# Kernel tuning notes

Measured on AMD Instinct MI355X. Metric: run time of the kernel, lower is better.

## Reference

```python
import jax, jax.numpy as jnp
import numpy as np

NODES_PER_GRAPH = 40
NEG_SLOPE = 0.1


def gcn_conv(x, src, dst, deg_inv_sqrt, W, b):
    # PyG GCNConv: h = x @ W.T; symmetric-normalized aggregation with self-loops; + bias
    h = x @ W.T                                   # [N, out]
    norm = deg_inv_sqrt[src] * deg_inv_sqrt[dst]  # [E]
    msgs = h[src] * norm[:, None]                 # [E, out]
    agg = jax.ops.segment_sum(msgs, dst, num_segments=x.shape[0])
    # self-loop contribution: norm_ii = deg_inv_sqrt[i]^2 = 1/deg[i]
    agg = agg + h * (deg_inv_sqrt ** 2)[:, None]
    return agg + b


def setup_inputs() -> dict:
    key = jax.random.key(0)
    ks = jax.random.split(key, 12)
    N, E, C = 200000, 1000000, 40
    hid1, hid2, hid3, lin1, lin2, out = 128, 256, 128, 512, 128, 1

    def glorot(k, shape):
        fan_in = shape[-1]
        return jax.random.normal(k, shape, dtype=jnp.float32) * (1.0 / np.sqrt(fan_in))

    x = jax.random.normal(ks[0], (N, C), dtype=jnp.float32)
    edge_index = jax.random.randint(ks[1], (2, E), 0, N, dtype=jnp.int64)
    return {
        "x": x,
        "edge_index": edge_index,
        "W1": glorot(ks[2], (hid1, C)), "b1": jnp.zeros((hid1,), jnp.float32),
        "W2": glorot(ks[3], (hid2, hid1)), "b2": jnp.zeros((hid2,), jnp.float32),
        "W3": glorot(ks[4], (hid3, hid2)), "b3": jnp.zeros((hid3,), jnp.float32),
        "L1w": glorot(ks[5], (lin1, NODES_PER_GRAPH * hid3)), "L1b": jnp.zeros((lin1,), jnp.float32),
        "L2w": glorot(ks[6], (lin2, lin1)), "L2b": jnp.zeros((lin2,), jnp.float32),
        "L3w": glorot(ks[7], (out, lin2)), "L3b": jnp.zeros((out,), jnp.float32),
    }


def reference(x, edge_index, W1, b1, W2, b2, W3, b3, L1w, L1b, L2w, L2b, L3w, L3b):
    N = x.shape[0]
    src, dst = edge_index[0], edge_index[1]
    # degree with self-loops (edge weight 1), shared by all three convs
    deg = jax.ops.segment_sum(jnp.ones_like(dst, dtype=x.dtype), dst, num_segments=N) + 1.0
    deg_inv_sqrt = jax.lax.rsqrt(deg)

    lrelu = lambda v: jax.nn.leaky_relu(v, NEG_SLOPE)

    h = lrelu(gcn_conv(x, src, dst, deg_inv_sqrt, W1, b1))
    # dropout is identity in eval mode
    h = lrelu(gcn_conv(h, src, dst, deg_inv_sqrt, W2, b2))
    h = lrelu(gcn_conv(h, src, dst, deg_inv_sqrt, W3, b3))

    g = h.reshape(N // NODES_PER_GRAPH, -1)   # [G, 40*hid3]
    g = lrelu(g @ L1w.T + L1b)
    g = lrelu(g @ L2w.T + L2b)
    g = g @ L3w.T + L3b
    return jax.nn.sigmoid(g)                   # [G, 1]
```

## Files before the change

### kernel.cpp

```cpp
#include <hip/hip_runtime.h>
#include <cmath>

#define CDIV(a,b) (((a)+(b)-1)/(b))

typedef unsigned short bf16_t;
using short8 = __attribute__((ext_vector_type(8))) short;
using f32x4  = __attribute__((ext_vector_type(4))) float;
using u16x4  = __attribute__((ext_vector_type(4))) unsigned short;
using u16x8  = __attribute__((ext_vector_type(8))) unsigned short;

__device__ __forceinline__ float bf2f(unsigned short b) {
    unsigned u = ((unsigned)b) << 16;
    float f;
    __builtin_memcpy(&f, &u, 4);
    return f;
}
__device__ __forceinline__ unsigned short f2bf(float f) {
    unsigned u;
    __builtin_memcpy(&u, &f, 4);
    u = (u + 0x7FFFu + ((u >> 16) & 1u)) >> 16;
    return (unsigned short)u;
}

__device__ __forceinline__ void gload16(const bf16_t* g, unsigned short* l) {
    __builtin_amdgcn_global_load_lds(
        (const __attribute__((address_space(1))) void*)(g),
        (__attribute__((address_space(3))) void*)(l), 16, 0, 0);
}

__device__ __forceinline__ int edge_src(const int* ei, int E, int f, int i) {
    return f ? ei[2 * (size_t)i] : ei[i];
}
__device__ __forceinline__ int edge_dst(const int* ei, int E, int f, int i) {
    return f ? ei[2 * ((size_t)E + (size_t)i)] : ei[(size_t)E + (size_t)i];
}

__global__ __launch_bounds__(256) void k_packhist(const int* __restrict__ ei, int E,
                                                  int* __restrict__ src32,
                                                  int* __restrict__ dst32,
                                                  int* __restrict__ cnt8, int N) {
    __shared__ int sflag;
    int t = threadIdx.x;
    if (t < 64) {
        unsigned v = (unsigned)ei[2 * t + 1];
        unsigned long long m = __ballot(v != 0u);
        if (t == 0) sflag = (m == 0ULL) ? 1 : 0;
    }
    __syncthreads();
    int i = blockIdx.x * 256 + t;
    if (i >= E) return;
    int f = sflag;
    int s = edge_src(ei, E, f, i);
    int d = edge_dst(ei, E, f, i);
    src32[i] = s;
    dst32[i] = d;
    if ((unsigned)d < (unsigned)N)
        atomicAdd(&cnt8[(blockIdx.x & 7) * N + d], 1);
}

__global__ void k_blockred(const int* __restrict__ cnt8, int* __restrict__ bsum, int N) {
    __shared__ int sd[256];
    int b = blockIdx.x, t = threadIdx.x;
    int base = b * 1024 + t * 4;
    int s = 0;
#pragma unroll
    for (int i = 0; i < 4; i++) {
        int idx = base + i;
        if (idx < N)
#pragma unroll
            for (int r = 0; r < 8; r++) s += cnt8[r * N + idx];
    }
    sd[t] = s; __syncthreads();
    for (int off = 128; off > 0; off >>= 1) { if (t < off) sd[t] += sd[t + off]; __syncthreads(); }
    if (t == 0) bsum[b] = sd[0];
}

__global__ void k_scanwrite(const int* __restrict__ cnt8, const int* __restrict__ bsum,
                            int* __restrict__ rowptr, int* __restrict__ cur,
                            float* __restrict__ dis, int N, int nb) {
    __shared__ int sb[256];
    __shared__ int sd[256];
    int b = blockIdx.x, t = threadIdx.x;
    int v0 = (t < nb) ? bsum[t] : 0;
    sb[t] = v0; __syncthreads();
    for (int off = 1; off < 256; off <<= 1) {
        int y = (t >= off) ? sb[t - off] : 0;
        __syncthreads();
        sb[t] += y;
        __syncthreads();
    }
    int block_pre = (b == 0) ? 0 : sb[b - 1];

    int base = b * 1024 + t * 4;
    int tot[4]; int s = 0;
#pragma unroll
    for (int i = 0; i < 4; i++) {
        int idx = base + i;
        tot[i] = 0;
        if (idx < N) {
#pragma unroll
            for (int r = 0; r < 8; r++) tot[i] += cnt8[r * N + idx];
        }
        s += tot[i];
    }
    sd[t] = s; __syncthreads();
    for (int off = 1; off < 256; off <<= 1) {
        int y = (t >= off) ? sd[t - off] : 0;
        __syncthreads();
        sd[t] += y;
        __syncthreads();
    }
    int pre = block_pre + sd[t] - s;
#pragma unroll
    for (int i = 0; i < 4; i++) {
        int idx = base + i;
        if (idx < N) {
            rowptr[idx] = pre;
            cur[idx] = pre;
            dis[idx] = rsqrtf((float)tot[i] + 1.0f);
            pre += tot[i];
        } else if (idx == N) {
            rowptr[N] = pre;
        }
    }
}

#define FILL_EPB 4096
__global__ __launch_bounds__(256) void k_fill_r(
        const int* __restrict__ src32, const int* __restrict__ dst32, int E,
        int* __restrict__ cur, int* __restrict__ csr, int N, int NR) {
    int r = blockIdx.x & 7;
    int chunk = blockIdx.x >> 3;
    int lo = r * NR;
    int hi = min(lo + NR, N);
    int base = chunk * FILL_EPB;
    int end = min(base + FILL_EPB, E);
    for (int i = base + threadIdx.x; i < end; i += 256) {
        int d = dst32[i];
        if (d >= lo && d < hi) {
            int s = src32[i];
            if ((unsigned)s < (unsigned)N) {
                int p = atomicAdd(&cur[d], 1);
                csr[p] = s;
            }
        }
    }
}


struct WcSeg { const float* src; bf16_t* dst; int M, KW, KP, nchunk; };

__global__ __launch_bounds__(256) void k_wconv(WcSeg s0, WcSeg s1, WcSeg s2,
                                               WcSeg s3, WcSeg s4, WcSeg s5,
                                               int wtotal, int* __restrict__ zdst,
                                               int total) {
    int i = blockIdx.x * 256 + threadIdx.x;
    if (i >= total) return;
    if (i >= wtotal) {
        int4 z = {0, 0, 0, 0};
        *(int4*)(zdst + (size_t)(i - wtotal) * 4) = z;
        return;
    }
    WcSeg s;
    if (i < s0.nchunk) s = s0;
    else if ((i -= s0.nchunk) < s1.nchunk) s = s1;
    else if ((i -= s1.nchunk) < s2.nchunk) s = s2;
    else if ((i -= s2.nchunk) < s3.nchunk) s = s3;
    else if ((i -= s3.nchunk) < s4.nchunk) s = s4;
    else { i -= s4.nchunk; s = s5; }
    int cpr = s.KP >> 3;
    int row = i / cpr, kk = (i % cpr) << 3;
    short8 v = {};
    if (kk < s.KW) {
        const float4* p = (const float4*)(s.src + (size_t)row * s.KW + kk);
        float4 a = p[0], b = p[1];
        v[0] = (short)f2bf(a.x); v[1] = (short)f2bf(a.y);
        v[2] = (short)f2bf(a.z); v[3] = (short)f2bf(a.w);
        v[4] = (short)f2bf(b.x); v[5] = (short)f2bf(b.y);
        v[6] = (short)f2bf(b.z); v[7] = (short)f2bf(b.w);
    }
    *(short8*)(s.dst + (size_t)row * s.KP + kk) = v;
}


template <bool CBF, bool BIAS, int ACT, bool SPLIT, bool SCALE>
__global__ __launch_bounds__(256) void gemm_mfma(
        const bf16_t* __restrict__ A, const bf16_t* __restrict__ Wb,
        const float* __restrict__ bias, void* __restrict__ Cv,
        int N, int K, int M, int Kseg, int nx, int ny,
        const float* __restrict__ rowscale) {
    constexpr int BM = 128, BK = 64;
    __shared__ __align__(16) unsigned short lds[4 * 64 * 68];
    unsigned short* Als = lds;
    unsigned short* Bls = lds + BM * BK;

    int t = threadIdx.x;
    int lane = t & 63, wid = t >> 6;
    int quad = lane >> 4, l15 = lane & 15;
    int wave_m = wid & 1, wave_n = wid >> 1;

    int bx, by, bz;
    if (SPLIT) {
        int bid = (int)blockIdx.x;
        int xcd = bid & 7, li = bid >> 3;
        bx = li % nx;
        int pl = li / nx;
        int ppx = (int)(gridDim.x >> 3) / nx;
        int pair = xcd * ppx + pl;
        by = pair % ny;
        bz = pair / ny;
    } else {
        bx = blockIdx.x; by = blockIdx.y; bz = 0;
    }

    int bm0 = by * BM;
    int bn0 = bx * BM;
    int kbeg = SPLIT ? bz * Kseg : 0;
    int kend = SPLIT ? min(kbeg + Kseg, K) : K;

    f32x4 acc[4][4] = {};

    for (int k0 = kbeg; k0 < kend; k0 += BK) {
#pragma unroll
        for (int it = 0; it < 4; it++) {
            int idx = t + it * 256;
            int row = idx >> 3, sc = idx & 7;
            int c = sc ^ (row & 7);
            int ga = bm0 + row; if (ga >= N) ga = N - 1;
            gload16(A + (size_t)ga * K + k0 + c * 8, Als + idx * 8);
            gload16(Wb + (size_t)(bn0 + row) * K + k0 + c * 8, Bls + idx * 8);
        }
        __syncthreads();

#pragma unroll
        for (int ks = 0; ks < 2; ks++) {
            short8 af[4], bfr[4];
            int ck = ks * 4 + quad;
            int sw = (ck ^ (l15 & 7)) << 3;
#pragma unroll
            for (int mt = 0; mt < 4; mt++)
                af[mt] = *(const short8*)&Als[(wave_m * 64 + mt * 16 + l15) * BK + sw];
#pragma unroll
            for (int nt = 0; nt < 4; nt++)
                bfr[nt] = *(const short8*)&Bls[(wave_n * 64 + nt * 16 + l15) * BK + sw];
#pragma unroll
            for (int mt = 0; mt < 4; mt++)
#pragma unroll
                for (int nt = 0; nt < 4; nt++)
                    acc[mt][nt] = __builtin_amdgcn_mfma_f32_16x16x32_bf16(
                        af[mt], bfr[nt], acc[mt][nt], 0, 0, 0);
        }
        __syncthreads();
    }

    if (!SPLIT && CBF) {
        constexpr int TST = 68;
        unsigned short* tw = lds + wid * 64 * TST;
#pragma unroll
        for (int mt = 0; mt < 4; mt++) {
#pragma unroll
            for (int nt = 0; nt < 4; nt++) {
                int tcol = nt * 16 + l15;
                float bv = BIAS ? bias[bn0 + wave_n * 64 + tcol] : 0.f;
#pragma unroll
                for (int r = 0; r < 4; r++) {
                    float x = acc[mt][nt][r];
                    if (BIAS) x += bv;
                    if (ACT == 1) x = x > 0.f ? x : 0.1f * x;
                    if (SCALE) {
                        int row = bm0 + wave_m * 64 + mt * 16 + quad * 4 + r;
                        x *= rowscale[row < N ? row : N - 1];
                    }
                    tw[(mt * 16 + quad * 4 + r) * TST + tcol] = f2bf(x);
                }
            }
        }
        __syncthreads();
        bf16_t* C = (bf16_t*)Cv;
        int lrow0 = lane >> 3, lcol = (lane & 7) * 8;
#pragma unroll
        for (int it = 0; it < 8; it++) {
            int lrow = it * 8 + lrow0;
            int row = bm0 + wave_m * 64 + lrow;
            if (row < N) {
                u16x8 v = *(const u16x8*)&tw[lrow * TST + lcol];
                *(u16x8*)&C[(size_t)row * M + bn0 + wave_n * 64 + lcol] = v;
            }
        }
    } else {
        float* Pz = SPLIT ? ((float*)Cv + (size_t)bz * N * M) : (float*)Cv;
#pragma unroll
        for (int mt = 0; mt < 4; mt++) {
            int rbase = bm0 + wave_m * 64 + mt * 16 + quad * 4;
#pragma unroll
            for (int nt = 0; nt < 4; nt++) {
                int col = bn0 + wave_n * 64 + nt * 16 + l15;
                float bv = (BIAS && !SPLIT) ? bias[col] : 0.f;
#pragma unroll
                for (int r = 0; r < 4; r++) {
                    int row = rbase + r;
                    if (row >= N) continue;
                    float x = acc[mt][nt][r];
                    if (!SPLIT) {
                        if (BIAS) x += bv;
                        if (ACT == 1) x = x > 0.f ? x : 0.1f * x;
                    }
                    Pz[(size_t)row * M + col] = x;
                }
            }
        }
    }
}

__global__ __launch_bounds__(256) void gemm_mlp2(
        const float* __restrict__ part6,
        const float* __restrict__ L1b,
        const bf16_t* __restrict__ Wb,
        float* __restrict__ Pout,
        int G) {
    constexpr int BM = 128, BK = 64, K = 512, M = 128, NY = 40;
    __shared__ __align__(16) unsigned short lds[2 * BM * BK];
    unsigned short* Als = lds;
    unsigned short* Bls = lds + BM * BK;

    int t = threadIdx.x;
    int lane = t & 63, wid = t >> 6;
    int quad = lane >> 4, l15 = lane & 15;
    int wave_m = wid & 1, wave_n = wid >> 1;

    int bid = (int)blockIdx.x;
    int xcd = bid & 7, li = bid >> 3;
    int ppx = (int)(gridDim.x >> 3);
    int pair = xcd * ppx + li;
    int by = pair % NY;
    int bz = pair / NY;

    int bm0 = by * BM;
    int kbeg = bz * (K / 4);
    size_t GK = (size_t)G * K;

    f32x4 acc[4][4] = {};

    for (int k0 = kbeg; k0 < kbeg + K / 4; k0 += BK) {
#pragma unroll
        for (int it = 0; it < 4; it++) {
            int idx = t + it * 256;
            int row = idx >> 3, sc = idx & 7;
            int cW = sc ^ (row & 7);
            gload16(Wb + (size_t)row * K + k0 + cW * 8, Bls + idx * 8);
            int g = bm0 + row; if (g >= G) g = G - 1;
            const float* pb = part6 + (size_t)g * K + k0 + sc * 8;
            float v[8] = {};
#pragma unroll
            for (int z = 0; z < 6; z++) {
                const float* pz = pb + (size_t)z * GK;
                float4 a = *(const float4*)pz;
                float4 b = *(const float4*)(pz + 4);
                v[0] += a.x; v[1] += a.y; v[2] += a.z; v[3] += a.w;
                v[4] += b.x; v[5] += b.y; v[6] += b.z; v[7] += b.w;
            }
            float4 b0 = *(const float4*)&L1b[k0 + sc * 8];
            float4 b1 = *(const float4*)&L1b[k0 + sc * 8 + 4];
            float bb[8] = {b0.x, b0.y, b0.z, b0.w, b1.x, b1.y, b1.z, b1.w};
            u16x8 o;
#pragma unroll
            for (int j = 0; j < 8; j++) {
                float xv = v[j] + bb[j];
                xv = xv > 0.f ? xv : 0.1f * xv;
                o[j] = f2bf(xv);
            }
            *(u16x8*)&Als[row * BK + ((sc ^ (row & 7)) << 3)] = o;
        }
        __syncthreads();

#pragma unroll
        for (int ks = 0; ks < 2; ks++) {
            short8 af[4], bfr[4];
            int ck = ks * 4 + quad;
            int sw = (ck ^ (l15 & 7)) << 3;
#pragma unroll
            for (int mt = 0; mt < 4; mt++)
                af[mt] = *(const short8*)&Als[(wave_m * 64 + mt * 16 + l15) * BK + sw];
#pragma unroll
            for (int nt = 0; nt < 4; nt++)
                bfr[nt] = *(const short8*)&Bls[(wave_n * 64 + nt * 16 + l15) * BK + sw];
#pragma unroll
            for (int mt = 0; mt < 4; mt++)
#pragma unroll
                for (int nt = 0; nt < 4; nt++)
                    acc[mt][nt] = __builtin_amdgcn_mfma_f32_16x16x32_bf16(
                        af[mt], bfr[nt], acc[mt][nt], 0, 0, 0);
        }
        __syncthreads();
    }

    float* Pz = Pout + (size_t)bz * G * M;
#pragma unroll
    for (int mt = 0; mt < 4; mt++) {
        int rbase = bm0 + wave_m * 64 + mt * 16 + quad * 4;
#pragma unroll
        for (int nt = 0; nt < 4; nt++) {
            int col = wave_n * 64 + nt * 16 + l15;
#pragma unroll
            for (int r = 0; r < 4; r++) {
                int row = rbase + r;
                if (row >= G) continue;
                Pz[(size_t)row * M + col] = acc[mt][nt][r];
            }
        }
    }
}

__global__ __launch_bounds__(256, 3) void gemm_fused23(
        const bf16_t* __restrict__ A,
        const bf16_t* __restrict__ W2,
        const float*  __restrict__ b2,
        const bf16_t* __restrict__ W3,
        const float*  __restrict__ dis,
        bf16_t* __restrict__ C,
        int N) {
    __shared__ __align__(16) unsigned short lds[24576];
    unsigned short* Als  = lds;
    unsigned short* Bls  = lds + 4096;
    unsigned short* H2ls = lds;
    unsigned short* B2ls = lds + 16384;

    int t = threadIdx.x;
    int lane = t & 63, wid = t >> 6;
    int quad = lane >> 4, l15 = lane & 15;
    int wm = wid & 1, wn = wid >> 1;
    int bm0 = blockIdx.x * 64;

    float bv[8];
#pragma unroll
    for (int nt = 0; nt < 8; nt++) bv[nt] = b2[wn * 128 + nt * 16 + l15];

    f32x4 acc1[2][8] = {};
    for (int k0 = 0; k0 < 128; k0 += 64) {
#pragma unroll
        for (int it = 0; it < 2; it++) {
            int idx = t + it * 256;
            int row = idx >> 3, sc = idx & 7;
            int c = sc ^ (row & 7);
            int g = bm0 + row; if (g >= N) g = N - 1;
            gload16(A + (size_t)g * 128 + k0 + c * 8, Als + idx * 8);
        }
#pragma unroll
        for (int it = 0; it < 8; it++) {
            int idx = t + it * 256;
            int row = idx >> 3, sc = idx & 7;
            int c = sc ^ (row & 7);
            gload16(W2 + (size_t)row * 128 + k0 + c * 8, Bls + idx * 8);
        }
        __syncthreads();
#pragma unroll
        for (int ks = 0; ks < 2; ks++) {
            int ck = ks * 4 + quad;
            int sw = (ck ^ (l15 & 7)) << 3;
            short8 af[2];
#pragma unroll
            for (int mt = 0; mt < 2; mt++)
                af[mt] = *(const short8*)&Als[(wm * 32 + mt * 16 + l15) * 64 + sw];
#pragma unroll
            for (int nt = 0; nt < 8; nt++) {
                short8 bfr = *(const short8*)&Bls[(wn * 128 + nt * 16 + l15) * 64 + sw];
#pragma unroll
                for (int mt = 0; mt < 2; mt++)
                    acc1[mt][nt] = __builtin_amdgcn_mfma_f32_16x16x32_bf16(
                        af[mt], bfr, acc1[mt][nt], 0, 0, 0);
            }
        }
        __syncthreads();
    }

#pragma unroll
    for (int it = 0; it < 4; it++) {
        int idx = t + it * 256;
        int row = idx >> 3, sc = idx & 7;
        int c = sc ^ (row & 7);
        gload16(W3 + (size_t)row * 256 + c * 8, B2ls + idx * 8);
    }

#pragma unroll
    for (int mt = 0; mt < 2; mt++) {
#pragma unroll
        for (int nt = 0; nt < 8; nt++) {
            int col = wn * 128 + nt * 16 + l15;
            int chunk = col >> 3, within = col & 7;
#pragma unroll
            for (int r = 0; r < 4; r++) {
                int row = wm * 32 + mt * 16 + quad * 4 + r;
                float xv = acc1[mt][nt][r] + bv[nt];
                xv = xv > 0.f ? xv : 0.1f * xv;
                H2ls[row * 256 + ((chunk ^ (row & 7)) << 3) + within] = f2bf(xv);
            }
        }
    }
    __syncthreads();

    f32x4 acc2[2][4] = {};
    for (int k0 = 0; k0 < 256; k0 += 64) {
        if (k0 > 0) {
#pragma unroll
            for (int it = 0; it < 4; it++) {
                int idx = t + it * 256;
                int row = idx >> 3, sc = idx & 7;
                int c = sc ^ (row & 7);
                gload16(W3 + (size_t)row * 256 + k0 + c * 8, B2ls + idx * 8);
            }
            __syncthreads();
        }
#pragma unroll
        for (int ks = 0; ks < 2; ks++) {
            int kc = (k0 >> 3) + ks * 4 + quad;
            int swa = (kc ^ (l15 & 7)) << 3;
            int swb = ((ks * 4 + quad) ^ (l15 & 7)) << 3;
            short8 af[2], bfr[4];
#pragma unroll
            for (int mt = 0; mt < 2; mt++)
                af[mt] = *(const short8*)&H2ls[(wm * 32 + mt * 16 + l15) * 256 + swa];
#pragma unroll
            for (int nt = 0; nt < 4; nt++)
                bfr[nt] = *(const short8*)&B2ls[(wn * 64 + nt * 16 + l15) * 64 + swb];
#pragma unroll
            for (int mt = 0; mt < 2; mt++)
#pragma unroll
                for (int nt = 0; nt < 4; nt++)
                    acc2[mt][nt] = __builtin_amdgcn_mfma_f32_16x16x32_bf16(
                        af[mt], bfr[nt], acc2[mt][nt], 0, 0, 0);
        }
        __syncthreads();
    }

    constexpr int TST = 68;
    unsigned short* tw = lds + wid * 32 * TST;
#pragma unroll
    for (int mt = 0; mt < 2; mt++) {
#pragma unroll
        for (int r = 0; r < 4; r++) {
            int row = bm0 + wm * 32 + mt * 16 + quad * 4 + r;
            float ds = dis[row < N ? row : N - 1];
#pragma unroll
            for (int nt = 0; nt < 4; nt++) {
                int tcol = nt * 16 + l15;
                tw[(mt * 16 + quad * 4 + r) * TST + tcol] = f2bf(acc2[mt][nt][r] * ds);
            }
        }
    }
    __syncthreads();
    int lrow0 = lane >> 3, lcol = (lane & 7) * 8;
#pragma unroll
    for (int it = 0; it < 4; it++) {
        int lrow = it * 8 + lrow0;
        int row = bm0 + wm * 32 + lrow;
        if (row < N) {
            u16x8 v = *(const u16x8*)&tw[lrow * TST + lcol];
            *(u16x8*)&C[(size_t)row * 128 + wn * 64 + lcol] = v;
        }
    }
}


template <int F, bool BACT, bool PRE>
__global__ __launch_bounds__(256) void k_agg(
        const bf16_t* __restrict__ H, const int* __restrict__ rowptr,
        const int* __restrict__ csr, const float* __restrict__ dis,
        const float* __restrict__ bias, bf16_t* __restrict__ out, int N) {
    constexpr int SUB = F / 8;
    constexpr int NPW = 64 / SUB;
    constexpr int SH  = (SUB == 16) ? 4 : 3;
    int gtid = blockIdx.x * 256 + threadIdx.x;
    int wave = gtid >> 6, lane = gtid & 63;
    int sub = lane >> SH, sl = lane & (SUB - 1);
    int node = wave * NPW + sub;
    if (node >= N) return;
    float di = dis[node];
    int s = rowptr[node], e = rowptr[node + 1];

    auto load_row = [&](const bf16_t* p, float (&r)[8]) {
        u16x8 v = *(const u16x8*)p;
#pragma unroll
        for (int f = 0; f < 8; f++) r[f] = bf2f(v[f]);
    };

    float acc[8], acc2[8];
    {
        float r[8];
        load_row(H + (size_t)node * F + sl * 8, r);
        float sln = PRE ? 1.f : di * di;
#pragma unroll
        for (int f = 0; f < 8; f++) { acc[f] = r[f] * sln; acc2[f] = 0.f; }
    }
    int p = s;
    for (; p + 4 <= e; p += 4) {
        int s0 = csr[p], s1 = csr[p + 1], s2 = csr[p + 2], s3 = csr[p + 3];
        float r0[8], r1[8], r2[8], r3[8];
        load_row(H + (size_t)s0 * F + sl * 8, r0);
        load_row(H + (size_t)s1 * F + sl * 8, r1);
        load_row(H + (size_t)s2 * F + sl * 8, r2);
        load_row(H + (size_t)s3 * F + sl * 8, r3);
        if (PRE) {
#pragma unroll
            for (int f = 0; f < 8; f++) {
                acc[f]  += r0[f] + r2[f];
                acc2[f] += r1[f] + r3[f];
            }
        } else {
            float n0 = dis[s0] * di, n1 = dis[s1] * di;
            float n2 = dis[s2] * di, n3 = dis[s3] * di;
#pragma unroll
            for (int f = 0; f < 8; f++) {
                acc[f]  += r0[f] * n0; acc2[f] += r1[f] * n1;
                acc[f]  += r2[f] * n2; acc2[f] += r3[f] * n3;
            }
        }
    }
    if (p + 2 <= e) {
        int s0 = csr[p], s1 = csr[p + 1];
        float r0[8], r1[8];
        load_row(H + (size_t)s0 * F + sl * 8, r0);
        load_row(H + (size_t)s1 * F + sl * 8, r1);
        if (PRE) {
#pragma unroll
            for (int f = 0; f < 8; f++) { acc[f] += r0[f]; acc2[f] += r1[f]; }
        } else {
            float n0 = dis[s0] * di, n1 = dis[s1] * di;
#pragma unroll
            for (int f = 0; f < 8; f++) { acc[f] += r0[f] * n0; acc2[f] += r1[f] * n1; }
        }
        p += 2;
    }
    if (p < e) {
        int s0 = csr[p];
        float r0[8];
        load_row(H + (size_t)s0 * F + sl * 8, r0);
        if (PRE) {
#pragma unroll
            for (int f = 0; f < 8; f++) acc[f] += r0[f];
        } else {
            float n0 = dis[s0] * di;
#pragma unroll
            for (int f = 0; f < 8; f++) acc[f] += r0[f] * n0;
        }
    }

    float o[8];
#pragma unroll
    for (int f = 0; f < 8; f++) {
        float v = acc[f] + acc2[f];
        if (PRE) v *= di;
        if (BACT) {
            v += bias[sl * 8 + f];
            v = v > 0.f ? v : 0.1f * v;
        }
        o[f] = v;
    }
    u16x8 w = {f2bf(o[0]), f2bf(o[1]), f2bf(o[2]), f2bf(o[3]),
               f2bf(o[4]), f2bf(o[5]), f2bf(o[6]), f2bf(o[7])};
    *(u16x8*)(out + (size_t)node * F + sl * 8) = w;
}


__global__ __launch_bounds__(256) void k_head2(
        const float* __restrict__ part, const float* __restrict__ L2b,
        const float* __restrict__ L3w, const float* __restrict__ L3b,
        float* __restrict__ out, int G) {
    int wv = (int)((blockIdx.x * blockDim.x + threadIdx.x) >> 6);
    int lane = threadIdx.x & 63;
    if (wv >= G) return;
    size_t base = (size_t)wv * 128 + lane * 2;
    size_t GM = (size_t)G * 128;
    float2 s = *(const float2*)&part[base];
#pragma unroll
    for (int z = 1; z < 4; z++) {
        float2 p = *(const float2*)&part[z * GM + base];
        s.x += p.x; s.y += p.y;
    }
    float2 b = *(const float2*)&L2b[lane * 2];
    float vx = s.x + b.x, vy = s.y + b.y;
    vx = vx > 0.f ? vx : 0.1f * vx;
    vy = vy > 0.f ? vy : 0.1f * vy;
    float2 wl = *(const float2*)&L3w[lane * 2];
    float d = vx * wl.x + vy * wl.y;
    for (int off = 32; off > 0; off >>= 1) d += __shfl_xor(d, off, 64);
    if (lane == 0) out[wv] = 1.f / (1.f + expf(-(d + L3b[0])));
}


extern "C" void kernel_launch(void* const* d_in, const int* in_sizes, int n_in,
                              void* d_out, int out_size, void* d_ws, size_t ws_size,
                              hipStream_t stream) {
    const float* x   = (const float*)d_in[0];
    const int*   ei  = (const int*)d_in[1];
    const float* W1  = (const float*)d_in[2];  const float* b1  = (const float*)d_in[3];
    const float* W2  = (const float*)d_in[4];  const float* b2  = (const float*)d_in[5];
    const float* W3  = (const float*)d_in[6];  const float* b3  = (const float*)d_in[7];
    const float* L1w = (const float*)d_in[8];  const float* L1b = (const float*)d_in[9];
    const float* L2w = (const float*)d_in[10]; const float* L2b = (const float*)d_in[11];
    const float* L3w = (const float*)d_in[12]; const float* L3b = (const float*)d_in[13];
    float* out = (float*)d_out;

    const int C = 40;
    const int N = in_sizes[0] / C;
    const int E = in_sizes[1] / 2;
    const int G = N / 40;
    const int H1d = 128, H2d = 256, H3d = 128, M1 = 512, M2 = 128;
    const int K1 = 40 * H3d;

    char* wsb = (char*)d_ws;
    size_t off = 0;
    auto alloc = [&](size_t bytes) -> void* {
        void* p = wsb + off;
        off += (bytes + 255) & ~(size_t)255;
        return p;
    };
    int*    cnt8   = (int*)alloc(4 * 8 * (size_t)N);
    int*    rowptr = (int*)alloc(4 * (size_t)(N + 1));
    int*    cur    = (int*)alloc(4 * (size_t)N);
    int*    csr    = (int*)alloc(4 * (size_t)E);
    int*    bsum   = (int*)alloc(4 * 512);
    float*  dis    = (float*)alloc(4 * (size_t)N);
    bf16_t* Hb     = (bf16_t*)alloc(2 * (size_t)N * H2d);
    bf16_t* Xb     = (bf16_t*)alloc(2 * (size_t)N * H2d);
    bf16_t* W1b    = (bf16_t*)alloc(2 * (size_t)H1d * 64);
    bf16_t* W2b    = (bf16_t*)alloc(2 * (size_t)H2d * H1d);
    bf16_t* W3b    = (bf16_t*)alloc(2 * (size_t)H3d * H2d);
    bf16_t* L1wb   = (bf16_t*)alloc(2 * (size_t)M1 * K1);
    bf16_t* L2wb   = (bf16_t*)alloc(2 * (size_t)M2 * M1);
    if (off > ws_size) return;

    int* src32 = (int*)Xb;
    int* dst32 = src32 + E;
    bf16_t* xb   = Hb;
    bf16_t* A1b  = Xb;
    bf16_t* H1   = Hb;
    bf16_t* A2   = Xb;
    bf16_t* H3p  = Xb;
    bf16_t* X3   = Hb;
    float*  part = (float*)Xb;
    float*  part2 = part + 6 * (size_t)G * M1;

    WcSeg s0 = {W1,  W1b,  H1d, 40,  64,  H1d * 64 / 8};
    WcSeg s1 = {W2,  W2b,  H2d, H1d, H1d, H2d * H1d / 8};
    WcSeg s2 = {W3,  W3b,  H3d, H2d, H2d, H3d * H2d / 8};
    WcSeg s3 = {L1w, L1wb, M1,  K1,  K1,  M1 * K1 / 8};
    WcSeg s4 = {L2w, L2wb, M2,  M1,  M1,  M2 * M1 / 8};
    WcSeg s5 = {x,   xb,   N,   40,  64,  N * 64 / 8};
    int wtotal = s0.nchunk + s1.nchunk + s2.nchunk + s3.nchunk + s4.nchunk + s5.nchunk;
    int ztotal = wtotal + 2 * N;
    k_wconv<<<CDIV(ztotal, 256), 256, 0, stream>>>(s0, s1, s2, s3, s4, s5,
                                                   wtotal, cnt8, ztotal);

    k_packhist<<<CDIV(E, 256), 256, 0, stream>>>(ei, E, src32, dst32, cnt8, N);
    int nb = CDIV(N + 1, 1024);
    k_blockred<<<nb, 256, 0, stream>>>(cnt8, bsum, N);
    k_scanwrite<<<nb, 256, 0, stream>>>(cnt8, bsum, rowptr, cur, dis, N, nb);
    int NR = CDIV(N, 8);
    k_fill_r<<<8 * CDIV(E, FILL_EPB), 256, 0, stream>>>(src32, dst32, E, cur, csr, N, NR);

    const int NB = CDIV(N, 128);

    k_agg<64, false, false><<<CDIV(N, 32), 256, 0, stream>>>(xb, rowptr, csr, dis, nullptr, A1b, N);
    gemm_mfma<true, true, 1, false, true><<<dim3(1, NB), 256, 0, stream>>>(A1b, W1b, b1, H1, N, 64, H1d, 0, 0, 0, dis);
    k_agg<128, false, true><<<CDIV(N, 16), 256, 0, stream>>>(H1, rowptr, csr, dis, nullptr, A2, N);
    gemm_fused23<<<CDIV(N, 64), 256, 0, stream>>>(A2, W2b, b2, W3b, dis, H3p, N);
    k_agg<128, true, true><<<CDIV(N, 16), 256, 0, stream>>>(H3p, rowptr, csr, dis, b3, X3, N);

    gemm_mfma<false, false, 0, true, false><<<960, 256, 0, stream>>>(X3, L1wb, nullptr, part, G, K1, M1, 896, 4, 40, nullptr);
    gemm_mlp2<<<160, 256, 0, stream>>>(part, L1b, L2wb, part2, G);
    k_head2<<<CDIV(G, 4), 256, 0, stream>>>(part2, L2b, L3w, L3b, out, G);
}
```

Measured before the change: 471.9 us.

## Fuse layer-2 neighbor aggregation into the fused GEMM2/3 kernel prologue

Removes the separate k_agg pass for layer 2 and instead gathers CSR neighbor rows of H1 directly inside gemm_fused23, writing the scaled bf16 aggregate into swizzled LDS as the A operand. This drops one kernel launch and the global write and re-read of the N×128 aggregated intermediate. In exchange the gather runs with 4 threads per row inside a GEMM kernel limited by launch bounds and LDS, which may lower memory-level parallelism for the irregular gather. The W2 tile load is also restructured into two halves so the full A tile can stay resident.

Measured after the change: 458.8 us. 1.03x faster.

```diff
diff --git a/kernel.cpp b/kernel.cpp
--- a/kernel.cpp
+++ b/kernel.cpp
@@ -412,16 +412,17 @@
 }
 
 __global__ __launch_bounds__(256, 3) void gemm_fused23(
-        const bf16_t* __restrict__ A,
+        const bf16_t* __restrict__ H1,
+        const int* __restrict__ rowptr, const int* __restrict__ csr,
+        const float* __restrict__ dis,
         const bf16_t* __restrict__ W2,
         const float*  __restrict__ b2,
         const bf16_t* __restrict__ W3,
-        const float*  __restrict__ dis,
         bf16_t* __restrict__ C,
         int N) {
     __shared__ __align__(16) unsigned short lds[24576];
     unsigned short* Als  = lds;
-    unsigned short* Bls  = lds + 4096;
+    unsigned short* Bls  = lds + 8192;
     unsigned short* H2ls = lds;
     unsigned short* B2ls = lds + 16384;
 
@@ -435,24 +436,83 @@
 #pragma unroll
     for (int nt = 0; nt < 8; nt++) bv[nt] = b2[wn * 128 + nt * 16 + l15];
 
+#pragma unroll
+    for (int it = 0; it < 8; it++) {
+        int idx = t + it * 256;
+        int row = idx >> 3, sc = idx & 7;
+        int c = sc ^ (row & 7);
+        gload16(W2 + (size_t)row * 128 + c * 8, Bls + idx * 8);
+    }
+
+    {
+        int r = t >> 2, l4 = t & 3;
+        int row = bm0 + r; if (row >= N) row = N - 1;
+        int cb = l4 * 32;
+        const bf16_t* Hrow = H1 + (size_t)row * 128 + cb;
+        float acc[32];
+        {
+            u16x8 v[4];
+#pragma unroll
+            for (int j = 0; j < 4; j++) v[j] = *(const u16x8*)(Hrow + j * 8);
+#pragma unroll
+            for (int j = 0; j < 4; j++)
+#pragma unroll
+                for (int f = 0; f < 8; f++) acc[j * 8 + f] = bf2f(v[j][f]);
+        }
+        int s = rowptr[row], e = rowptr[row + 1];
+        int p = s;
+        for (; p + 2 <= e; p += 2) {
+            int s0 = csr[p], s1 = csr[p + 1];
+            const bf16_t* p0 = H1 + (size_t)s0 * 128 + cb;
+            const bf16_t* p1 = H1 + (size_t)s1 * 128 + cb;
+            u16x8 a0[4], a1[4];
+#pragma unroll
+            for (int j = 0; j < 4; j++) { a0[j] = *(const u16x8*)(p0 + j * 8);
+                                          a1[j] = *(const u16x8*)(p1 + j * 8); }
+#pragma unroll
+            for (int j = 0; j < 4; j++)
+#pragma unroll
+                for (int f = 0; f < 8; f++)
+                    acc[j * 8 + f] += bf2f(a0[j][f]) + bf2f(a1[j][f]);
+        }
+        if (p < e) {
+            int s0 = csr[p];
+            const bf16_t* p0 = H1 + (size_t)s0 * 128 + cb;
+            u16x8 a0[4];
+#pragma unroll
+            for (int j = 0; j < 4; j++) a0[j] = *(const u16x8*)(p0 + j * 8);
+#pragma unroll
+            for (int j = 0; j < 4; j++)
+#pragma unroll
+                for (int f = 0; f < 8; f++) acc[j * 8 + f] += bf2f(a0[j][f]);
+        }
+        float di = dis[row];
+#pragma unroll
+        for (int j = 0; j < 4; j++) {
+            int col0 = cb + j * 8;
+            int h = col0 >> 6;
+            int ck = (col0 & 63) >> 3;
+            int swc = ck ^ (r & 7);
+            u16x8 o;
+#pragma unroll
+            for (int f = 0; f < 8; f++) o[f] = f2bf(acc[j * 8 + f] * di);
+            *(u16x8*)&Als[h * 4096 + r * 64 + (swc << 3)] = o;
+        }
+    }
+    __syncthreads();
+
     f32x4 acc1[2][8] = {};
-    for (int k0 = 0; k0 < 128; k0 += 64) {
-#pragma unroll
-        for (int it = 0; it < 2; it++) {
-            int idx = t + it * 256;
-            int row = idx >> 3, sc = idx & 7;
-            int c = sc ^ (row & 7);
-            int g = bm0 + row; if (g >= N) g = N - 1;
-            gload16(A + (size_t)g * 128 + k0 + c * 8, Als + idx * 8);
-        }
-#pragma unroll
-        for (int it = 0; it < 8; it++) {
-            int idx = t + it * 256;
-            int row = idx >> 3, sc = idx & 7;
-            int c = sc ^ (row & 7);
-            gload16(W2 + (size_t)row * 128 + k0 + c * 8, Bls + idx * 8);
-        }
-        __syncthreads();
+    for (int h = 0; h < 2; h++) {
+        if (h > 0) {
+#pragma unroll
+            for (int it = 0; it < 8; it++) {
+                int idx = t + it * 256;
+                int row = idx >> 3, sc = idx & 7;
+                int c = sc ^ (row & 7);
+                gload16(W2 + (size_t)row * 128 + 64 + c * 8, Bls + idx * 8);
+            }
+            __syncthreads();
+        }
 #pragma unroll
         for (int ks = 0; ks < 2; ks++) {
             int ck = ks * 4 + quad;
@@ -460,7 +520,7 @@
             short8 af[2];
 #pragma unroll
             for (int mt = 0; mt < 2; mt++)
-                af[mt] = *(const short8*)&Als[(wm * 32 + mt * 16 + l15) * 64 + sw];
+                af[mt] = *(const short8*)&Als[h * 4096 + (wm * 32 + mt * 16 + l15) * 64 + sw];
 #pragma unroll
             for (int nt = 0; nt < 8; nt++) {
                 short8 bfr = *(const short8*)&Bls[(wn * 128 + nt * 16 + l15) * 64 + sw];
@@ -734,7 +794,6 @@
     bf16_t* xb   = Hb;
     bf16_t* A1b  = Xb;
     bf16_t* H1   = Hb;
-    bf16_t* A2   = Xb;
     bf16_t* H3p  = Xb;
     bf16_t* X3   = Hb;
     float*  part = (float*)Xb;
@@ -762,8 +821,7 @@
 
     k_agg<64, false, false><<<CDIV(N, 32), 256, 0, stream>>>(xb, rowptr, csr, dis, nullptr, A1b, N);
     gemm_mfma<true, true, 1, false, true><<<dim3(1, NB), 256, 0, stream>>>(A1b, W1b, b1, H1, N, 64, H1d, 0, 0, 0, dis);
-    k_agg<128, false, true><<<CDIV(N, 16), 256, 0, stream>>>(H1, rowptr, csr, dis, nullptr, A2, N);
-    gemm_fused23<<<CDIV(N, 64), 256, 0, stream>>>(A2, W2b, b2, W3b, dis, H3p, N);
+    gemm_fused23<<<CDIV(N, 64), 256, 0, stream>>>(H1, rowptr, csr, dis, W2b, b2, W3b, H3p, N);
     k_agg<128, true, true><<<CDIV(N, 16), 256, 0, stream>>>(H3p, rowptr, csr, dis, b3, X3, N);
 
     gemm_mfma<false, false, 0, true, false><<<960, 256, 0, stream>>>(X3, L1wb, nullptr, part, G, K1, M1, 896, 4, 40, nullptr);
```
